# Performance work log

Hardware: AMD Instinct MI355X
Metric: run time of the kernel (lower is better)

Reference implementation:

```python
import jax, jax.numpy as jnp
import numpy as np
from jax import lax

NB = 8        # nbands
BS = 32       # block_size
MTF = 41      # MTF kernel size
N = BS * BS   # self.N = block_size**2


def _dwconv(x, k):
    # depthwise (groups=NB) VALID conv, NCHW / OIHW
    return lax.conv_general_dilated(
        x, k, window_strides=(1, 1), padding='VALID',
        dimension_numbers=('NCHW', 'OIHW', 'NCHW'),
        feature_group_count=NB)


def setup_inputs() -> dict:
    key = jax.random.key(0)
    k1, k2, k3 = jax.random.split(key, 3)
    outputs = jax.random.normal(k1, (4, NB, 552, 552), dtype=jnp.float32)
    labels = jax.random.normal(k2, (4, NB, 512, 512), dtype=jnp.float32)
    # frozen per-band MTF lowpass kernel (requires_grad=False in the original)
    mtf_kernel = jax.random.normal(k3, (NB, 1, MTF, MTF), dtype=jnp.float32) * 0.02
    return {"outputs": outputs, "labels": labels, "mtf_kernel": mtf_kernel}


def reference(outputs, labels, mtf_kernel):
    box = jnp.ones((NB, 1, BS, BS), dtype=jnp.float32)  # all-ones box kernel
    o = _dwconv(outputs, mtf_kernel)                    # [4,NB,512,512]
    # five box-sum (moving window sum) maps -> [4,NB,481,481]
    o_sum = _dwconv(o, box)
    l_sum = _dwconv(labels, box)
    o_sq_sum = _dwconv(o * o, box)
    l_sq_sum = _dwconv(labels * labels, box)
    ol_sum = _dwconv(o * labels, box)

    mul = o_sum * l_sum                     # outputs_labels_sum_mul
    sq = o_sum ** 2 + l_sum ** 2            # outputs_labels_sum_mul_sq
    numerator = 4.0 * (N * ol_sum - mul) * mul
    denom_temp = N * (o_sq_sum + l_sq_sum) - sq
    denominator = denom_temp * sq

    quality_map = jnp.ones_like(denominator)
    idx1 = (denom_temp == 0) & (sq != 0)
    quality_map = jnp.where(idx1, 2.0 * mul / jnp.where(idx1, sq, 1.0), quality_map)
    idx2 = denominator != 0
    quality_map = jnp.where(idx2, numerator / jnp.where(idx2, denominator, 1.0), quality_map)

    return 1.0 - jnp.mean(quality_map)
```

## Files before the change

kernel.cpp:

```cpp
#include <hip/hip_runtime.h>

#define NBANDS 8
#define BS 32
#define MTF 41
#define IMG 552
#define CONV 512
#define QOUT 481
#define NIMG 32
#define NN 1024.0f

#define TX 560
#define TY 576

typedef _Float16 half8 __attribute__((ext_vector_type(8)));
typedef float f32x16 __attribute__((ext_vector_type(16)));

__global__ __launch_bounds__(256) void prep_transpose(
    const float* __restrict__ in, _Float16* __restrict__ T)
{
    __shared__ _Float16 s[64][72];
    int bid = blockIdx.x;
    int img = bid / 81;
    int t = bid % 81;
    int ty = t / 9, tx2 = t % 9;
    int y0 = ty * 64, x0 = tx2 * 64;
    const float* ip = in + (size_t)img * IMG * IMG;

    for (int k = 0; k < 16; ++k) {
        int i = k * 256 + threadIdx.x;
        int r = i >> 6, c = i & 63;
        int y = y0 + r, x = x0 + c;
        float v = (y < IMG && x < IMG) ? ip[(size_t)y * IMG + x] : 0.f;
        s[c][r] = (_Float16)v;
    }
    __syncthreads();
    _Float16* Tp = T + (size_t)img * TX * TY;
    for (int k = 0; k < 2; ++k) {
        int i = k * 256 + threadIdx.x;
        int xi = i >> 3, g = i & 7;
        int x = x0 + xi;
        if (x < TX) {
            half8 v = *(const half8*)&s[xi][g * 8];
            *(half8*)&Tp[(size_t)x * TY + y0 + g * 8] = v;
        }
    }
}

__global__ __launch_bounds__(320) void prep_atab32(
    const float* __restrict__ w, _Float16* __restrict__ A)
{
    int bid = blockIdx.x;
    int band = bid / MTF, kx = bid % MTF;
    int s = threadIdx.x >> 6, lane = threadIdx.x & 63;
    int i = lane & 31;
    int kb = 16 * s + ((lane >> 5) << 3);
    const float* wp = w + band * MTF * MTF;
    half8 v;
#pragma unroll
    for (int j = 0; j < 8; ++j) {
        int ky = kb + j - i;
        v[j] = (ky >= 0 && ky < MTF) ? (_Float16)wp[ky * MTF + kx] : (_Float16)0.f;
    }
    *(half8*)&A[(((size_t)bid * 5 + s) << 9) + lane * 8] = v;
}

#define XP2 168

__global__ __launch_bounds__(256, 4) void conv_mfma64x(
    const _Float16* __restrict__ T, const _Float16* __restrict__ Atab,
    float* __restrict__ out)
{
    extern __shared__ _Float16 sB[];
    int bid = blockIdx.x;
    int img = bid >> 5;
    int rr  = bid & 31;
    int yb  = rr >> 2, xb = rr & 3;
    int y0 = yb << 6;
    int x0 = xb << 7;
    int band = img & 7;
    int tid = threadIdx.x;

    const _Float16* Tp = T + (size_t)img * TX * TY;
    for (int e = tid; e < 14 * XP2; e += 256) {
        int g = e / XP2, x = e - g * XP2;
        half8 v = *(const half8*)&Tp[(size_t)(x0 + x) * TY + y0 + g * 8];
        *(half8*)&sB[(size_t)e * 8] = v;
    }
    __syncthreads();

    int l  = tid & 63;
    int wx = tid >> 6;
    int l5 = l >> 5;
    int ln = l & 31;

    const half8* Ab = (const half8*)(Atab + (((size_t)band * MTF * 5) << 9)) + l;
    int base = l5 * XP2 + ln + (wx << 5);

    f32x16 a0 = {}, a1 = {};

    auto LDA = [&](half8 (&A)[5], int kx) {
        const half8* q = Ab + (size_t)kx * 5 * 64;
#pragma unroll
        for (int s = 0; s < 5; ++s) A[s] = q[(size_t)s * 64];
    };

    auto body = [&](half8 (&A)[5], int kx) {
        const char* p = (const char*)sB + ((size_t)(base + kx) << 4);
        half8 B[7];
#pragma unroll
        for (int b = 0; b < 7; ++b) B[b] = *(const half8*)(p + b * (2 * XP2 * 16));
#pragma unroll
        for (int s = 0; s < 5; ++s) {
            a0 = __builtin_amdgcn_mfma_f32_32x32x16_f16(A[s], B[s],     a0, 0, 0, 0);
            a1 = __builtin_amdgcn_mfma_f32_32x32x16_f16(A[s], B[s + 2], a1, 0, 0, 0);
        }
    };

    half8 A0[5], A1[5];
    LDA(A0, 0);
#pragma unroll 1
    for (int kx = 0; kx < 40; kx += 2) {
        LDA(A1, kx + 1);
        body(A0, kx);
        LDA(A0, kx + 2);
        body(A1, kx + 1);
    }
    body(A0, 40);

    float* op = out + (size_t)img * CONV * CONV;
    int colb = x0 + (wx << 5) + ln;
    int rb   = y0 + (l5 << 2);
#pragma unroll
    for (int r2 = 0; r2 < 16; ++r2) {
        int rowo = (r2 & 3) + ((r2 >> 2) << 3);
        op[(size_t)(rb + rowo) * CONV + colb]      = a0[r2];
        op[(size_t)(rb + 32 + rowo) * CONV + colb] = a1[r2];
    }
}

template<int C, int RM, int BM, bool BC>
__device__ __forceinline__ float dppadd(float v) {
    int t = __builtin_amdgcn_update_dpp(0, __builtin_bit_cast(int, v), C, RM, BM, BC);
    return v + __builtin_bit_cast(float, t);
}

__device__ __forceinline__ float wave_iscan(float v) {
    v = dppadd<0x111, 0xf, 0xf, true >(v);
    v = dppadd<0x112, 0xf, 0xf, true >(v);
    v = dppadd<0x114, 0xf, 0xf, true >(v);
    v = dppadd<0x118, 0xf, 0xf, true >(v);
    v = dppadd<0x142, 0xa, 0xf, false>(v);
    v = dppadd<0x143, 0xc, 0xf, false>(v);
    return v;
}

__device__ __forceinline__ float win32(float s, int lane) {
    float P = wave_iscan(s);
    float Pg = __shfl(P, lane + 31, 64);
    return Pg - P + s;
}

__device__ __forceinline__ float qval(float A0, float A1, float A2, float A3) {
    float mul = A0 * A1;
    float sq  = fmaf(A0, A0, A1 * A1);
    float num = 4.f * fmaf(NN, A3, -mul) * mul;
    float dt  = fmaf(NN, A2, -sq);
    float den = dt * sq;
    bool  c1  = (dt == 0.f) && (sq != 0.f);
    float nn = num, dd = den;
    if (den == 0.f) { nn = c1 ? 2.f * mul : 1.f; dd = c1 ? sq : 1.f; }
    return nn * __builtin_amdgcn_rcpf(dd);
}

__global__ __launch_bounds__(512) void box_q_wave2(
    const float* __restrict__ o,
    const float* __restrict__ lab,
    double* __restrict__ acc)
{
    int bid  = blockIdx.x;
    int img  = bid >> 4;
    int rr   = bid & 15;
    int pair = rr >> 1;
    int xblk = rr & 1;
    int wid  = threadIdx.x >> 6;
    int lane = threadIdx.x & 63;

    int c0 = xblk * 256 + wid * 32;
    int c  = c0 + lane;
    bool cvalid = c < CONV;
    int r0A = pair * 62;
    int r0B = r0A + 31;
    int nB  = min(31, QOUT - r0B);

    const float* op = o   + (size_t)img * CONV * CONV + c;
    const float* lp = lab + (size_t)img * CONV * CONV + c;

    float sA0=0,sA1=0,sA2=0,sA3=0, sB0=0,sB1=0,sB2=0,sB3=0;
#pragma unroll 2
    for (int k = 0; k < BS; ++k) {
        float ov=0, lv=0, ow=0, lw=0;
        if (cvalid) {
            ov = op[(size_t)(r0A + k) * CONV]; lv = lp[(size_t)(r0A + k) * CONV];
            ow = op[(size_t)(r0B + k) * CONV]; lw = lp[(size_t)(r0B + k) * CONV];
        }
        sA0 += ov; sA1 += lv;
        sA2 = fmaf(ov, ov, fmaf(lv, lv, sA2)); sA3 = fmaf(ov, lv, sA3);
        sB0 += ow; sB1 += lw;
        sB2 = fmaf(ow, ow, fmaf(lw, lw, sB2)); sB3 = fmaf(ow, lw, sB3);
    }

    int x = c0 + lane;
    bool xvalid = (lane < 32) && (x < QOUT);
    float qacc = 0.f;

#pragma unroll 1
    for (int i = 0; i < 31; ++i) {
        bool mA = (i < 30), mB = (i + 1 < nB);
        float oa=0,la2=0,ob=0,lb=0, oc=0,lc=0,od=0,ld=0;
        if (mA && cvalid) {
            oa = op[(size_t)(r0A + i + BS) * CONV]; la2 = lp[(size_t)(r0A + i + BS) * CONV];
            ob = op[(size_t)(r0A + i) * CONV];      lb  = lp[(size_t)(r0A + i) * CONV];
        }
        if (mB && cvalid) {
            oc = op[(size_t)(r0B + i + BS) * CONV]; lc = lp[(size_t)(r0B + i + BS) * CONV];
            od = op[(size_t)(r0B + i) * CONV];      ld = lp[(size_t)(r0B + i) * CONV];
        }

        {
            float A0 = win32(sA0, lane), A1 = win32(sA1, lane);
            float A2 = win32(sA2, lane), A3 = win32(sA3, lane);
            if (xvalid) qacc += qval(A0, A1, A2, A3);
        }
        if (i < nB) {
            float B0 = win32(sB0, lane), B1 = win32(sB1, lane);
            float B2 = win32(sB2, lane), B3 = win32(sB3, lane);
            if (xvalid) qacc += qval(B0, B1, B2, B3);
        }

        sA0 += oa - ob; sA1 += la2 - lb;
        sA2 = fmaf(oa, oa, fmaf(la2, la2, fmaf(ob, -ob, fmaf(lb, -lb, sA2))));
        sA3 = fmaf(oa, la2, fmaf(ob, -lb, sA3));
        sB0 += oc - od; sB1 += lc - ld;
        sB2 = fmaf(oc, oc, fmaf(lc, lc, fmaf(od, -od, fmaf(ld, -ld, sB2))));
        sB3 = fmaf(oc, lc, fmaf(od, -ld, sB3));
    }

    qacc += __shfl_down(qacc, 16, 64);
    qacc += __shfl_down(qacc, 8, 64);
    qacc += __shfl_down(qacc, 4, 64);
    qacc += __shfl_down(qacc, 2, 64);
    qacc += __shfl_down(qacc, 1, 64);
    if (lane == 0) atomicAdd(&acc[img], (double)qacc);
}

__global__ void finalize_kernel(const double* __restrict__ acc, float* __restrict__ out)
{
    double t = 0.0;
    for (int i = 0; i < NIMG; ++i) t += acc[i];
    out[0] = 1.0f - (float)(t / 7403552.0);
}

extern "C" void kernel_launch(void* const* d_in, const int* in_sizes, int n_in,
                              void* d_out, int out_size, void* d_ws, size_t ws_size,
                              hipStream_t stream)
{
    const float* outputs = (const float*)d_in[0];
    const float* labels  = (const float*)d_in[1];
    const float* mtf     = (const float*)d_in[2];

    double*    acc   = (double*)d_ws;
    float*     o_buf = (float*)((char*)d_ws + 4096);
    _Float16*  T     = (_Float16*)((char*)d_ws + 4096 + 33554432);
    _Float16*  Atab  = (_Float16*)((char*)d_ws + 4096 + 33554432 + 20643840);

    hipMemsetAsync(d_ws, 0, 256, stream);

    prep_transpose<<<NIMG * 81, 256, 0, stream>>>(outputs, T);
    prep_atab32<<<NBANDS * MTF, 320, 0, stream>>>(mtf, Atab);
    conv_mfma64x<<<NIMG * 32, 256, 14 * XP2 * 16, stream>>>(T, Atab, o_buf);
    box_q_wave2<<<NIMG * 16, 512, 0, stream>>>(o_buf, labels, acc);
    finalize_kernel<<<1, 1, 0, stream>>>(acc, (float*)d_out);
}
```

Measured before the change: 142.8 us.

## Split box-quality kernel into one strip per wave and triple-buffer conv A loads

```diff
diff --git a/kernel.cpp b/kernel.cpp
--- a/kernel.cpp
+++ b/kernel.cpp
@@ -66,7 +66,7 @@
 
 #define XP2 168
 
-__global__ __launch_bounds__(256, 4) void conv_mfma64x(
+__global__ __launch_bounds__(256, 3) void conv_mfma64x(
     const _Float16* __restrict__ T, const _Float16* __restrict__ Atab,
     float* __restrict__ out)
 {
@@ -116,16 +116,20 @@
         }
     };
 
-    half8 A0[5], A1[5];
+    half8 A0[5], A1[5], A2[5];
     LDA(A0, 0);
+    LDA(A1, 1);
 #pragma unroll 1
-    for (int kx = 0; kx < 40; kx += 2) {
-        LDA(A1, kx + 1);
+    for (int kx = 0; kx < 39; kx += 3) {
+        LDA(A2, kx + 2);
         body(A0, kx);
-        LDA(A0, kx + 2);
+        LDA(A0, kx + 3);
         body(A1, kx + 1);
-    }
-    body(A0, 40);
+        LDA(A1, kx + 4);
+        body(A2, kx + 2);
+    }
+    body(A0, 39);
+    body(A1, 40);
 
     float* op = out + (size_t)img * CONV * CONV;
     int colb = x0 + (wx << 5) + ln;
@@ -172,41 +176,37 @@
     return nn * __builtin_amdgcn_rcpf(dd);
 }
 
-__global__ __launch_bounds__(512) void box_q_wave2(
+#define SROWS 31
+
+__global__ __launch_bounds__(256) void box_q_wave1(
     const float* __restrict__ o,
     const float* __restrict__ lab,
     double* __restrict__ acc)
 {
-    int bid  = blockIdx.x;
-    int img  = bid >> 4;
-    int rr   = bid & 15;
-    int pair = rr >> 1;
-    int xblk = rr & 1;
-    int wid  = threadIdx.x >> 6;
-    int lane = threadIdx.x & 63;
-
-    int c0 = xblk * 256 + wid * 32;
+    int bid   = blockIdx.x;
+    int img   = bid >> 6;
+    int strip = (bid >> 2) & 15;
+    int xblk  = bid & 3;
+    int wid   = threadIdx.x >> 6;
+    int lane  = threadIdx.x & 63;
+
+    int c0 = xblk * 128 + wid * 32;
     int c  = c0 + lane;
     bool cvalid = c < CONV;
-    int r0A = pair * 62;
-    int r0B = r0A + 31;
-    int nB  = min(31, QOUT - r0B);
+    int r0 = strip * SROWS;
+    int nrows = min(SROWS, QOUT - r0);
 
     const float* op = o   + (size_t)img * CONV * CONV + c;
     const float* lp = lab + (size_t)img * CONV * CONV + c;
 
-    float sA0=0,sA1=0,sA2=0,sA3=0, sB0=0,sB1=0,sB2=0,sB3=0;
-#pragma unroll 2
-    for (int k = 0; k < BS; ++k) {
-        float ov=0, lv=0, ow=0, lw=0;
-        if (cvalid) {
-            ov = op[(size_t)(r0A + k) * CONV]; lv = lp[(size_t)(r0A + k) * CONV];
-            ow = op[(size_t)(r0B + k) * CONV]; lw = lp[(size_t)(r0B + k) * CONV];
-        }
-        sA0 += ov; sA1 += lv;
-        sA2 = fmaf(ov, ov, fmaf(lv, lv, sA2)); sA3 = fmaf(ov, lv, sA3);
-        sB0 += ow; sB1 += lw;
-        sB2 = fmaf(ow, ow, fmaf(lw, lw, sB2)); sB3 = fmaf(ow, lw, sB3);
+    float s0 = 0.f, s1 = 0.f, s2 = 0.f, s3 = 0.f;
+#pragma unroll 4
+    for (int r = r0; r < r0 + BS; ++r) {
+        float ov = cvalid ? op[(size_t)r * CONV] : 0.f;
+        float lv = cvalid ? lp[(size_t)r * CONV] : 0.f;
+        s0 += ov; s1 += lv;
+        s2 = fmaf(ov, ov, fmaf(lv, lv, s2));
+        s3 = fmaf(ov, lv, s3);
     }
 
     int x = c0 + lane;
@@ -214,35 +214,27 @@
     float qacc = 0.f;
 
 #pragma unroll 1
-    for (int i = 0; i < 31; ++i) {
-        bool mA = (i < 30), mB = (i + 1 < nB);
-        float oa=0,la2=0,ob=0,lb=0, oc=0,lc=0,od=0,ld=0;
-        if (mA && cvalid) {
-            oa = op[(size_t)(r0A + i + BS) * CONV]; la2 = lp[(size_t)(r0A + i + BS) * CONV];
-            ob = op[(size_t)(r0A + i) * CONV];      lb  = lp[(size_t)(r0A + i) * CONV];
+    for (int i = 0;; ++i) {
+        float oa = 0.f, la = 0.f, ob = 0.f, lb = 0.f;
+        bool more = (i + 1 < nrows);
+        if (more && cvalid) {
+            int radd = r0 + i + BS, rsub = r0 + i;
+            oa = op[(size_t)radd * CONV]; la = lp[(size_t)radd * CONV];
+            ob = op[(size_t)rsub * CONV]; lb = lp[(size_t)rsub * CONV];
         }
-        if (mB && cvalid) {
-            oc = op[(size_t)(r0B + i + BS) * CONV]; lc = lp[(size_t)(r0B + i + BS) * CONV];
-            od = op[(size_t)(r0B + i) * CONV];      ld = lp[(size_t)(r0B + i) * CONV];
-        }
-
-        {
-            float A0 = win32(sA0, lane), A1 = win32(sA1, lane);
-            float A2 = win32(sA2, lane), A3 = win32(sA3, lane);
-            if (xvalid) qacc += qval(A0, A1, A2, A3);
-        }
-        if (i < nB) {
-            float B0 = win32(sB0, lane), B1 = win32(sB1, lane);
-            float B2 = win32(sB2, lane), B3 = win32(sB3, lane);
-            if (xvalid) qacc += qval(B0, B1, B2, B3);
-        }
-
-        sA0 += oa - ob; sA1 += la2 - lb;
-        sA2 = fmaf(oa, oa, fmaf(la2, la2, fmaf(ob, -ob, fmaf(lb, -lb, sA2))));
-        sA3 = fmaf(oa, la2, fmaf(ob, -lb, sA3));
-        sB0 += oc - od; sB1 += lc - ld;
-        sB2 = fmaf(oc, oc, fmaf(lc, lc, fmaf(od, -od, fmaf(ld, -ld, sB2))));
-        sB3 = fmaf(oc, lc, fmaf(od, -ld, sB3));
+
+        float A0 = win32(s0, lane);
+        float A1 = win32(s1, lane);
+        float A2 = win32(s2, lane);
+        float A3 = win32(s3, lane);
+
+        if (xvalid) qacc += qval(A0, A1, A2, A3);
+
+        if (!more) break;
+        s0 += oa - ob;
+        s1 += la - lb;
+        s2 = fmaf(oa, oa, fmaf(la, la, fmaf(ob, -ob, fmaf(lb, -lb, s2))));
+        s3 = fmaf(oa, la, fmaf(ob, -lb, s3));
     }
 
     qacc += __shfl_down(qacc, 16, 64);
@@ -278,6 +270,6 @@
     prep_transpose<<<NIMG * 81, 256, 0, stream>>>(outputs, T);
     prep_atab32<<<NBANDS * MTF, 320, 0, stream>>>(mtf, Atab);
     conv_mfma64x<<<NIMG * 32, 256, 14 * XP2 * 16, stream>>>(T, Atab, o_buf);
-    box_q_wave2<<<NIMG * 16, 512, 0, stream>>>(o_buf, labels, acc);
+    box_q_wave1<<<NIMG * 64, 256, 0, stream>>>(o_buf, labels, acc);
     finalize_kernel<<<1, 1, 0, stream>>>(acc, (float*)d_out);
 }
```

Measured after the change: 168.7 us. +18.1%, slower.
